# Optimization experiments

Measured on AMD Instinct MI355X. Metric: run time of the kernel, lower is better.

Reference implementation:

```python
import jax, jax.numpy as jnp
import numpy as np

B, S, H, NH = 2, 2048, 4096, 32
D = H // NH  # head_dim = 128
ROPE_THETA = 10000.0


def setup_inputs() -> dict:
    key = jax.random.key(0)
    k0, k1, k2 = jax.random.split(key, 3)
    hidden_states = jax.random.normal(k0, (B, S, H), dtype=jnp.float32) * 0.02
    w_pack = jax.random.normal(k1, (H, 3 * H), dtype=jnp.float32) * 0.02  # fused QKV weight
    w_o = jax.random.normal(k2, (H, H), dtype=jnp.float32) * 0.02         # o_proj weight
    positions = jnp.broadcast_to(jnp.arange(S, dtype=jnp.int32), (B, S))
    return {"positions": positions, "hidden_states": hidden_states, "w_pack": w_pack, "w_o": w_o}


def _rope(x, positions):
    # neox-style rotary embedding (vLLM get_rope default), x: [B, S, NH, D]
    half = D // 2
    inv_freq = 1.0 / (ROPE_THETA ** (jnp.arange(0, half, dtype=jnp.float32) * 2.0 / D))
    freqs = positions.astype(jnp.float32)[..., None] * inv_freq  # [B, S, half]
    cos = jnp.cos(freqs)[:, :, None, :]  # [B, S, 1, half]
    sin = jnp.sin(freqs)[:, :, None, :]
    x1, x2 = x[..., :half], x[..., half:]
    return jnp.concatenate([x1 * cos - x2 * sin, x2 * cos + x1 * sin], axis=-1)


def reference(positions, hidden_states, w_pack, w_o):
    # fused QKV projection
    qkv = jnp.einsum('bsh,hf->bsf', hidden_states, w_pack)
    q, k, v = jnp.split(qkv, 3, axis=-1)
    q = q.reshape(B, S, NH, D)
    k = k.reshape(B, S, NH, D)
    v = v.reshape(B, S, NH, D)
    # RoPE on q, k
    q = _rope(q, positions)
    k = _rope(k, positions)
    # causal scaled dot-product attention
    scale = D ** -0.5
    scores = jnp.einsum('bqhd,bkhd->bhqk', q, k) * scale  # [B, NH, S, S]
    causal = jnp.tril(jnp.ones((S, S), dtype=bool))
    scores = jnp.where(causal[None, None], scores, jnp.finfo(scores.dtype).min)
    probs = jax.nn.softmax(scores, axis=-1)
    out = jnp.einsum('bhqk,bkhd->bqhd', probs, v).reshape(B, S, H)
    # output projection
    return jnp.einsum('bsh,hf->bsf', out, w_o)
```

## Files before the change

### kernel.cpp

```cpp
#include <hip/hip_runtime.h>

#define Sdim   2048
#define Hdim   4096
#define NHEADS 32
#define Dh     128
#define Mrows  4096
#define QKVLD  12288

typedef __attribute__((ext_vector_type(8))) short short8;
typedef __attribute__((ext_vector_type(4))) float f32x4;
typedef __attribute__((ext_vector_type(4))) float float4v;

__device__ __forceinline__ short f2bf(float f) {
  union { float f; unsigned u; } x; x.f = f;
  unsigned r = x.u + 0x7fffu + ((x.u >> 16) & 1u);
  return (short)(r >> 16);
}
__device__ __forceinline__ float bf2f(short s) {
  union { unsigned u; float f; } x; x.u = ((unsigned)(unsigned short)s) << 16;
  return x.f;
}

__device__ __forceinline__ void gload_lds16(const void* g, void* l) {
  __builtin_amdgcn_global_load_lds(
      (const __attribute__((address_space(1))) void*)g,
      (__attribute__((address_space(3))) void*)l, 16, 0, 0);
}

__global__ void k_cvt(const float* __restrict__ src, short* __restrict__ dst, int n8) {
  int idx = blockIdx.x * blockDim.x + threadIdx.x;
  if (idx >= n8) return;
  const float4v* s = (const float4v*)src + (size_t)idx * 2;
  float4v a = s[0], b = s[1];
  short8 o;
  o[0] = f2bf(a.x); o[1] = f2bf(a.y); o[2] = f2bf(a.z); o[3] = f2bf(a.w);
  o[4] = f2bf(b.x); o[5] = f2bf(b.y); o[6] = f2bf(b.z); o[7] = f2bf(b.w);
  *((short8*)dst + idx) = o;
}

__global__ void k_tcvt64(const float* __restrict__ src, short* __restrict__ dst,
                         int R, int C) {
  __shared__ float t[64][65];
  const int tid = threadIdx.x;
  const int r0 = blockIdx.y * 64, c0 = blockIdx.x * 64;
  const int ir = tid >> 4, ic = (tid & 15) << 2;
#pragma unroll
  for (int p = 0; p < 4; ++p) {
    const float4v v = *(const float4v*)(src + (size_t)(r0 + p * 16 + ir) * C + c0 + ic);
    t[p * 16 + ir][ic] = v.x; t[p * 16 + ir][ic + 1] = v.y;
    t[p * 16 + ir][ic + 2] = v.z; t[p * 16 + ir][ic + 3] = v.w;
  }
  __syncthreads();
  const int oc = tid >> 3, orr = (tid & 7) << 3;
#pragma unroll
  for (int p = 0; p < 2; ++p) {
    int c = p * 32 + oc;
    short8 o;
#pragma unroll
    for (int j = 0; j < 8; ++j) o[j] = f2bf(t[orr + j][c]);
    *(short8*)(dst + (size_t)(c0 + c) * R + r0 + orr) = o;
  }
}

__device__ __forceinline__ void stage_half256(const short* G, int ld, int row0, int kcol,
                                              char* lds, int tid) {
#pragma unroll
  for (int j = 0; j < 2; ++j) {
    int p = j * 512 + tid;
    int r = p >> 3;
    int c = ((p & 7) ^ (r & 7)) << 3;
    gload_lds16(G + (size_t)(row0 + r) * ld + kcol + c,
                lds + ((j * 512 + (tid & 448)) << 4));
  }
}

#define MFMA_Q(qm, qn)                                                                   \
  do {                                                                                   \
    __builtin_amdgcn_s_setprio(1);                                                       \
    _Pragma("unroll")                                                                    \
    for (int m4 = 0; m4 < 4; ++m4)                                                       \
      _Pragma("unroll")                                                                  \
      for (int n2 = 0; n2 < 2; ++n2) {                                                   \
        acc[(qm)*4+m4][(qn)*2+n2] = __builtin_amdgcn_mfma_f32_16x16x32_bf16(             \
            av[m4][0], bv[(qn)*2+n2][0], acc[(qm)*4+m4][(qn)*2+n2], 0, 0, 0);            \
        acc[(qm)*4+m4][(qn)*2+n2] = __builtin_amdgcn_mfma_f32_16x16x32_bf16(             \
            av[m4][1], bv[(qn)*2+n2][1], acc[(qm)*4+m4][(qn)*2+n2], 0, 0, 0);            \
      }                                                                                  \
    __builtin_amdgcn_s_setprio(0);                                                       \
  } while (0)

#define PH_BARRIER()                    \
  do {                                  \
    __builtin_amdgcn_s_barrier();       \
    __builtin_amdgcn_sched_barrier(0);  \
  } while (0)

template<bool C_F32>
__global__ __launch_bounds__(512, 2) void k_gemm256(const short* __restrict__ A, int lda,
                                                    const short* __restrict__ Bt, int ldb,
                                                    void* __restrict__ Cp, int ldc,
                                                    int Ndim, int Kdim) {
  __shared__ __align__(16) char smem[131072];
  const int tid  = threadIdx.x;
  const int lane = tid & 63;
  const int wave = tid >> 6;
  const int lo = lane & 15, hi = lane >> 4;
  const int wr = wave >> 2, wc = wave & 3;

  const int nblk = gridDim.x;
  const int lid = (blockIdx.x & 7) * (nblk >> 3) + (blockIdx.x >> 3);
  const int nbn = Ndim >> 8;
  const int bm0 = (lid / nbn) << 8;
  const int bn0 = (lid % nbn) << 8;

  f32x4 acc[8][4];
#pragma unroll
  for (int i = 0; i < 8; ++i)
#pragma unroll
    for (int j = 0; j < 4; ++j) acc[i][j] = (f32x4){0.f, 0.f, 0.f, 0.f};

  short8 av[4][2], bv[4][2];
  const int swz = (lo & 7) << 4;
  const int brow = (wc & 1) * 64;

  stage_half256(Bt, ldb, bn0,       0, smem + 32768,         tid);
  stage_half256(Bt, ldb, bn0 + 128, 0, smem + 32768 + 16384, tid);
  stage_half256(A,  lda, bm0,       0, smem,                 tid);
  stage_half256(A,  lda, bm0 + 128, 0, smem + 16384,         tid);

  const int NK = Kdim >> 6;
  for (int kt = 0; kt < NK; ++kt) {
    const int cur = kt & 1;
    const char* Ab = smem + cur * 65536 + wr * 16384;
    const char* Bb = smem + cur * 65536 + 32768 + (wc >> 1) * 16384;
    char* nA = smem + (cur ^ 1) * 65536;
    char* nB = nA + 32768;
    const int kc = (kt + 1) << 6;
    const bool pf = (kt + 1 < NK);

    if (pf) {
      stage_half256(Bt, ldb, bn0,       kc, nB,         tid);
      stage_half256(Bt, ldb, bn0 + 128, kc, nB + 16384, tid);
      asm volatile("s_waitcnt vmcnt(4)" ::: "memory");
    } else {
      asm volatile("s_waitcnt vmcnt(0)" ::: "memory");
    }
    PH_BARRIER();
#pragma unroll
    for (int m4 = 0; m4 < 4; ++m4)
#pragma unroll
      for (int ks = 0; ks < 2; ++ks)
        av[m4][ks] = *(const short8*)(Ab + (m4 * 16 + lo) * 128 + ((ks * 64 + hi * 16) ^ swz));
#pragma unroll
    for (int ni = 0; ni < 2; ++ni)
#pragma unroll
      for (int ks = 0; ks < 2; ++ks)
        bv[ni][ks] = *(const short8*)(Bb + (brow + ni * 16 + lo) * 128 + ((ks * 64 + hi * 16) ^ swz));
    MFMA_Q(0, 0);
#pragma unroll
    for (int ni = 2; ni < 4; ++ni)
#pragma unroll
      for (int ks = 0; ks < 2; ++ks)
        bv[ni][ks] = *(const short8*)(Bb + (brow + ni * 16 + lo) * 128 + ((ks * 64 + hi * 16) ^ swz));

    if (pf) {
      stage_half256(A, lda, bm0,       kc, nA,         tid);
      stage_half256(A, lda, bm0 + 128, kc, nA + 16384, tid);
    }
    PH_BARRIER();
    MFMA_Q(0, 1);
#pragma unroll
    for (int m4 = 0; m4 < 4; ++m4)
#pragma unroll
      for (int ks = 0; ks < 2; ++ks)
        av[m4][ks] = *(const short8*)(Ab + ((64 + m4 * 16 + lo) * 128) + ((ks * 64 + hi * 16) ^ swz));

    PH_BARRIER();
    MFMA_Q(1, 0);

    PH_BARRIER();
    MFMA_Q(1, 1);
  }

#pragma unroll
  for (int mi = 0; mi < 8; ++mi)
#pragma unroll
    for (int r = 0; r < 4; ++r) {
      int row = bm0 + wr * 128 + mi * 16 + hi * 4 + r;
#pragma unroll
      for (int ni = 0; ni < 4; ++ni) {
        int col = bn0 + wc * 64 + ni * 16 + lo;
        if (C_F32) ((float*)Cp)[(size_t)row * ldc + col] = acc[mi][ni][r];
        else       ((short*)Cp)[(size_t)row * ldc + col] = f2bf(acc[mi][ni][r]);
      }
    }
}

__global__ void k_ropevt(short* __restrict__ qkv, const int* __restrict__ positions,
                         short* __restrict__ vt) {
  __shared__ short tile[4096];
  const int bid = blockIdx.x;
  const int tid = threadIdx.x;
  if (bid < 4096) {
    int idx = bid * 256 + tid;
    int t = idx & 7;
    int h = (idx >> 3) & 31;
    int row = idx >> 8;
    float pos = (float)positions[row];
    size_t o = (size_t)row * QKVLD + h * 128 + t * 8;
    short8 q1 = *(short8*)(qkv + o),        q2 = *(short8*)(qkv + o + 64);
    short8 k1 = *(short8*)(qkv + o + 4096), k2 = *(short8*)(qkv + o + 4160);
#pragma unroll
    for (int j = 0; j < 8; ++j) {
      int d = t * 8 + j;
      float inv = exp2f((float)d * -0.2076205059304570f);
      float ang = pos * inv, s, c;
      sincosf(ang, &s, &c);
      float a1 = bf2f(q1[j]), a2 = bf2f(q2[j]);
      q1[j] = f2bf(a1 * c - a2 * s); q2[j] = f2bf(a2 * c + a1 * s);
      float b1 = bf2f(k1[j]), b2 = bf2f(k2[j]);
      k1[j] = f2bf(b1 * c - b2 * s); k2[j] = f2bf(b2 * c + b1 * s);
    }
    *(short8*)(qkv + o) = q1;        *(short8*)(qkv + o + 64) = q2;
    *(short8*)(qkv + o + 4096) = k1; *(short8*)(qkv + o + 4160) = k2;
  } else {
    int idx = bid - 4096;
    const int c0 = (idx & 63) << 6;
    const int s0 = ((idx >> 6) & 31) << 6;
    const int b  = idx >> 11;
#pragma unroll
    for (int j = 0; j < 2; ++j) {
      int chunk = j * 256 + tid;
      int row = chunk >> 3, c8 = chunk & 7;
      short8 v = *(const short8*)(qkv + (size_t)(b * 2048 + s0 + row) * QKVLD + 8192 + c0 + c8 * 8);
      int sw = c8 ^ ((row ^ (row >> 3)) & 7);
      *(short8*)((char*)tile + row * 128 + sw * 16) = v;
    }
    __syncthreads();
#pragma unroll
    for (int j = 0; j < 2; ++j) {
      int chunk = j * 256 + tid;
      int d = chunk >> 3, s8 = (chunk & 7) << 3;
      short8 o;
#pragma unroll
      for (int j2 = 0; j2 < 8; ++j2) {
        int s = s8 + j2;
        int sw = ((d >> 3) ^ ((s ^ (s >> 3)) & 7));
        o[j2] = *(const short*)((const char*)tile + s * 128 + sw * 16 + (d & 7) * 2);
      }
      *(short8*)(vt + (size_t)(b * 4096 + c0 + d) * Sdim + s0 + s8) = o;
    }
  }
}

__device__ __forceinline__ void stage_kv(const short* Kb, const short* Vtb, int kv0,
                                         char* kbuf, char* vbuf, int tid, int wave) {
#pragma unroll
  for (int i = 0; i < 4; ++i) {
    int p = i * 256 + tid;
    int r = p >> 4;
    int c = (p & 15) ^ (r & 7);
    gload_lds16(Kb + (size_t)(kv0 + r) * QKVLD + (c << 3),
                kbuf + ((i * 256 + wave * 64) << 4));
  }
#pragma unroll
  for (int i = 0; i < 4; ++i) {
    int p = i * 256 + tid;
    int r = p >> 3;
    int c = (p & 7) ^ (r & 7);
    gload_lds16(Vtb + (size_t)r * Sdim + kv0 + (c << 3),
                vbuf + ((i * 256 + wave * 64) << 4));
  }
}

__global__ __launch_bounds__(256, 2) void k_attn(short* __restrict__ qkv,
                                                 const short* __restrict__ Vt,
                                                 const float* __restrict__ w_o,
                                                 short* __restrict__ Wot) {
  __shared__ __align__(16) char smem[81920];
  const int tid  = threadIdx.x;

  if (blockIdx.x >= 1024) {
    float (*t)[65] = (float(*)[65])smem;
    const int idx = blockIdx.x - 1024;
    const int c0 = (idx & 63) << 6, r0 = (idx >> 6) << 6;
    const int ir = tid >> 4, ic = (tid & 15) << 2;
#pragma unroll
    for (int p = 0; p < 4; ++p) {
      const float4v v = *(const float4v*)(w_o + (size_t)(r0 + p * 16 + ir) * 4096 + c0 + ic);
      t[p * 16 + ir][ic] = v.x; t[p * 16 + ir][ic + 1] = v.y;
      t[p * 16 + ir][ic + 2] = v.z; t[p * 16 + ir][ic + 3] = v.w;
    }
    __syncthreads();
    const int oc = tid >> 3, orr = (tid & 7) << 3;
#pragma unroll
    for (int p = 0; p < 2; ++p) {
      int c = p * 32 + oc;
      short8 o;
#pragma unroll
      for (int j = 0; j < 8; ++j) o[j] = f2bf(t[orr + j][c]);
      *(short8*)(Wot + (size_t)(c0 + c) * 4096 + r0 + orr) = o;
    }
    return;
  }

  const int lane = tid & 63;
  const int wave = tid >> 6;
  const int lo = lane & 15, hi = lane >> 4;

  const int bid = blockIdx.x;
  const int lid = (bid & 7) * 128 + (bid >> 3);
  const int bh = lid >> 4;
  const int qt = 15 - (lid & 15);
  const int b = bh >> 5, h = bh & 31;
  const int q0 = qt << 7;

  short* base = qkv + (size_t)b * Sdim * QKVLD;
  const short* Qb = base + h * Dh;
  const short* Kb = base + Hdim + h * Dh;
  const short* Vtb = Vt + (size_t)(b * 32 + h) * 128 * Sdim;
  const int qrow0 = q0 + wave * 32;

  short* Pw = (short*)(smem + 65536 + wave * 4096);

  const float SEXP = 0.088388347648318447f * 1.4426950408889634f;

  short8 qf[2][4];
#pragma unroll
  for (int mi = 0; mi < 2; ++mi)
#pragma unroll
    for (int ks = 0; ks < 4; ++ks) {
      qf[mi][ks] = *(const short8*)(Qb + (size_t)(qrow0 + mi * 16 + lo) * QKVLD + ks * 32 + hi * 8);
#pragma unroll
      for (int j = 0; j < 8; ++j)
        qf[mi][ks][j] = f2bf(bf2f(qf[mi][ks][j]) * SEXP);
    }

  f32x4 acc_o[2][9];
  float m_run[2][4];
#pragma unroll
  for (int mi = 0; mi < 2; ++mi) {
#pragma unroll
    for (int nf = 0; nf < 9; ++nf) acc_o[mi][nf] = (f32x4){0.f, 0.f, 0.f, 0.f};
#pragma unroll
    for (int r = 0; r < 4; ++r) m_run[mi][r] = -1e30f;
  }

  short8 vones;
#pragma unroll
  for (int j = 0; j < 8; ++j) vones[j] = (short)0x3F80;

  const int nkv = (q0 + 128) >> 6;
  const int swz = (lo & 7) << 4;

  stage_kv(Kb, Vtb, 0, smem, smem + 16384, tid, wave);
  __syncthreads();

  int cur = 0;
  for (int kvt = 0; kvt < nkv; ++kvt) {
    const int kv0 = kvt << 6;
    if (kvt + 1 < nkv)
      stage_kv(Kb, Vtb, kv0 + 64, smem + (cur ^ 1) * 32768,
               smem + (cur ^ 1) * 32768 + 16384, tid, wave);

    if (kv0 <= qrow0 + 31) {
      const char* kl = smem + cur * 32768;
      const char* vl = smem + cur * 32768 + 16384;

      f32x4 accs[2][4];
#pragma unroll
      for (int mi = 0; mi < 2; ++mi)
#pragma unroll
        for (int nf = 0; nf < 4; ++nf) accs[mi][nf] = (f32x4){0.f, 0.f, 0.f, 0.f};
#pragma unroll
      for (int ks = 0; ks < 4; ++ks) {
        short8 kf[4];
#pragma unroll
        for (int nf = 0; nf < 4; ++nf) {
          int r = nf * 16 + lo;
          kf[nf] = *(const short8*)(kl + r * 256 + ((ks * 64 + hi * 16) ^ swz));
        }
        __builtin_amdgcn_s_setprio(1);
#pragma unroll
        for (int mi = 0; mi < 2; ++mi)
#pragma unroll
          for (int nf = 0; nf < 4; ++nf)
            accs[mi][nf] = __builtin_amdgcn_mfma_f32_16x16x32_bf16(qf[mi][ks], kf[nf], accs[mi][nf], 0, 0, 0);
        __builtin_amdgcn_s_setprio(0);
      }

      const bool needmask = (kv0 + 63 > qrow0);
      float pmax[2][4];
      bool okall = true;
#pragma unroll
      for (int mi = 0; mi < 2; ++mi) {
#pragma unroll
        for (int r = 0; r < 4; ++r) {
          const int qrow = qrow0 + mi * 16 + hi * 4 + r;
          if (needmask) {
#pragma unroll
            for (int nf = 0; nf < 4; ++nf) {
              int col = kv0 + nf * 16 + lo;
              accs[mi][nf][r] = (col <= qrow) ? accs[mi][nf][r] : -1e30f;
            }
          }
          float tmax = fmaxf(fmaxf(accs[mi][0][r], accs[mi][1][r]),
                             fmaxf(accs[mi][2][r], accs[mi][3][r]));
#pragma unroll
          for (int off = 1; off < 16; off <<= 1)
            tmax = fmaxf(tmax, __shfl_xor(tmax, off, 64));
          pmax[mi][r] = tmax;
          okall = okall && (tmax <= m_run[mi][r] + 8.0f);
        }
      }
      if (!__all(okall)) {
#pragma unroll
        for (int mi = 0; mi < 2; ++mi)
#pragma unroll
          for (int r = 0; r < 4; ++r) {
            float mnew = fmaxf(m_run[mi][r], pmax[mi][r]);
            float alpha = exp2f(m_run[mi][r] - mnew);
            m_run[mi][r] = mnew;
#pragma unroll
            for (int nf = 0; nf < 9; ++nf) acc_o[mi][nf][r] *= alpha;
          }
      }
#pragma unroll
      for (int mi = 0; mi < 2; ++mi)
#pragma unroll
        for (int r = 0; r < 4; ++r) {
          const int prow = mi * 16 + hi * 4 + r;
          const int psw = prow & 7;
#pragma unroll
          for (int nf = 0; nf < 4; ++nf) {
            float p = exp2f(accs[mi][nf][r] - m_run[mi][r]);
            int col = nf * 16 + lo;
            Pw[(prow << 6) + (((col >> 3) ^ psw) << 3) + (col & 7)] = f2bf(p);
          }
        }

#pragma unroll
      for (int ks = 0; ks < 2; ++ks) {
        short8 pf[2];
#pragma unroll
        for (int mi = 0; mi < 2; ++mi) {
          int prow = mi * 16 + lo;
          pf[mi] = *(const short8*)((const char*)Pw + prow * 128 + (((ks * 4 + hi) ^ (prow & 7)) << 4));
        }
        __builtin_amdgcn_s_setprio(1);
#pragma unroll
        for (int nf = 0; nf < 9; ++nf) {
          short8 vf;
          if (nf < 8) {
            int row = nf * 16 + lo;
            vf = *(const short8*)(vl + row * 128 + ((ks * 64 + hi * 16) ^ swz));
          } else {
            vf = vones;
          }
#pragma unroll
          for (int mi = 0; mi < 2; ++mi)
            acc_o[mi][nf] = __builtin_amdgcn_mfma_f32_16x16x32_bf16(pf[mi], vf, acc_o[mi][nf], 0, 0, 0);
        }
        __builtin_amdgcn_s_setprio(0);
      }
    }

    __syncthreads();
    cur ^= 1;
  }

  short* Osm = (short*)smem;
#pragma unroll
  for (int mi = 0; mi < 2; ++mi)
#pragma unroll
    for (int r = 0; r < 4; ++r) {
      float inv = 1.0f / acc_o[mi][8][r];
      int row = wave * 32 + mi * 16 + hi * 4 + r;
#pragma unroll
      for (int nf = 0; nf < 8; ++nf)
        Osm[row * 128 + nf * 16 + lo] = f2bf(acc_o[mi][nf][r] * inv);
    }
  __syncthreads();
  short* Ob = base + h * Dh;
#pragma unroll
  for (int it = 0; it < 8; ++it) {
    int chunk = it * 256 + tid;
    int row = chunk >> 4, c8 = chunk & 15;
    *(short8*)(Ob + (size_t)(q0 + row) * QKVLD + c8 * 8) =
        *(const short8*)(Osm + row * 128 + c8 * 8);
  }
}

extern "C" void kernel_launch(void* const* d_in, const int* in_sizes, int n_in,
                              void* d_out, int out_size, void* d_ws, size_t ws_size,
                              hipStream_t stream) {
  const int*   positions = (const int*)d_in[0];
  const float* hidden    = (const float*)d_in[1];
  const float* w_pack    = (const float*)d_in[2];
  const float* w_o       = (const float*)d_in[3];
  float* out = (float*)d_out;

  char* ws = (char*)d_ws;
  short* Wpt  = (short*)ws;
  short* qkvb = (short*)(ws + (size_t)12288 * 4096 * 2);
  short* Wot  = (short*)ws;
  short* Hbf  = (short*)d_out;
  short* Vtg  = (short*)((char*)d_out + ((size_t)32 << 20));

  k_cvt<<<8192, 256, 0, stream>>>(hidden, Hbf, 4096 * 4096 / 8);
  k_tcvt64<<<dim3(12288 / 64, 4096 / 64), 256, 0, stream>>>(w_pack, Wpt, 4096, 12288);
  k_gemm256<false><<<dim3(768), 512, 0, stream>>>(Hbf, 4096, Wpt, 4096, qkvb, QKVLD, 12288, 4096);
  k_ropevt<<<8192, 256, 0, stream>>>(qkvb, positions, Vtg);
  k_attn<<<dim3(5120), 256, 0, stream>>>(qkvb, Vtg, w_o, Wot);
  k_gemm256<true><<<dim3(256), 512, 0, stream>>>(qkvb, QKVLD, Wot, 4096, out, 4096, 4096, 4096);
}
```

Before: 744.8 us.

## Fuse RoPE and V transpose into the QKV GEMM epilogue

Removes the separate RoPE/V-transpose kernel. The QKV GEMM now applies the rotary embedding in its epilogue and writes V transposed straight to the Vt buffer. To make this possible, each wave's B-tile column mapping changes so that a lane holds the d and d+64 pair of a head together. This saves a full read-modify-write pass over the qkv buffer and one kernel launch. In exchange, the transposed V stores are strided 8-byte writes, the epilogue adds sincos work, and the changed column interleave may affect LDS bank behaviour.

```diff
diff --git a/kernel.cpp b/kernel.cpp
--- a/kernel.cpp
+++ b/kernel.cpp
@@ -8,6 +8,7 @@
 #define QKVLD  12288
 
 typedef __attribute__((ext_vector_type(8))) short short8;
+typedef __attribute__((ext_vector_type(4))) short short4v;
 typedef __attribute__((ext_vector_type(4))) float f32x4;
 typedef __attribute__((ext_vector_type(4))) float float4v;
 
@@ -95,11 +96,13 @@
     __builtin_amdgcn_sched_barrier(0);  \
   } while (0)
 
-template<bool C_F32>
+template<int MODE>
 __global__ __launch_bounds__(512, 2) void k_gemm256(const short* __restrict__ A, int lda,
                                                     const short* __restrict__ Bt, int ldb,
                                                     void* __restrict__ Cp, int ldc,
-                                                    int Ndim, int Kdim) {
+                                                    int Ndim, int Kdim,
+                                                    const int* __restrict__ positions,
+                                                    short* __restrict__ Vtg) {
   __shared__ __align__(16) char smem[131072];
   const int tid  = threadIdx.x;
   const int lane = tid & 63;
@@ -121,7 +124,6 @@
 
   short8 av[4][2], bv[4][2];
   const int swz = (lo & 7) << 4;
-  const int brow = (wc & 1) * 64;
 
   stage_half256(Bt, ldb, bn0,       0, smem + 32768,         tid);
   stage_half256(Bt, ldb, bn0 + 128, 0, smem + 32768 + 16384, tid);
@@ -132,7 +134,7 @@
   for (int kt = 0; kt < NK; ++kt) {
     const int cur = kt & 1;
     const char* Ab = smem + cur * 65536 + wr * 16384;
-    const char* Bb = smem + cur * 65536 + 32768 + (wc >> 1) * 16384;
+    const char* Bb = smem + cur * 65536 + 32768;
     char* nA = smem + (cur ^ 1) * 65536;
     char* nB = nA + 32768;
     const int kc = (kt + 1) << 6;
@@ -155,13 +157,13 @@
     for (int ni = 0; ni < 2; ++ni)
 #pragma unroll
       for (int ks = 0; ks < 2; ++ks)
-        bv[ni][ks] = *(const short8*)(Bb + (brow + ni * 16 + lo) * 128 + ((ks * 64 + hi * 16) ^ swz));
+        bv[ni][ks] = *(const short8*)(Bb + (wc * 16 + ni * 64 + lo) * 128 + ((ks * 64 + hi * 16) ^ swz));
     MFMA_Q(0, 0);
 #pragma unroll
     for (int ni = 2; ni < 4; ++ni)
 #pragma unroll
       for (int ks = 0; ks < 2; ++ks)
-        bv[ni][ks] = *(const short8*)(Bb + (brow + ni * 16 + lo) * 128 + ((ks * 64 + hi * 16) ^ swz));
+        bv[ni][ks] = *(const short8*)(Bb + (wc * 16 + ni * 64 + lo) * 128 + ((ks * 64 + hi * 16) ^ swz));
 
     if (pf) {
       stage_half256(A, lda, bm0,       kc, nA,         tid);
@@ -182,74 +184,52 @@
     MFMA_Q(1, 1);
   }
 
-#pragma unroll
-  for (int mi = 0; mi < 8; ++mi)
-#pragma unroll
-    for (int r = 0; r < 4; ++r) {
-      int row = bm0 + wr * 128 + mi * 16 + hi * 4 + r;
+  if (MODE == 0) {
+#pragma unroll
+    for (int mi = 0; mi < 8; ++mi)
+#pragma unroll
+      for (int r = 0; r < 4; ++r) {
+        int row = bm0 + wr * 128 + mi * 16 + hi * 4 + r;
+#pragma unroll
+        for (int ni = 0; ni < 4; ++ni) {
+          int col = bn0 + wc * 16 + ni * 64 + lo;
+          ((float*)Cp)[(size_t)row * ldc + col] = acc[mi][ni][r];
+        }
+      }
+  } else if (bn0 < 8192) {
+    short* qkvb = (short*)Cp;
+    const int dd = wc * 16 + lo;
+    const float inv = exp2f((float)dd * -0.2076205059304570f);
+#pragma unroll
+    for (int mi = 0; mi < 8; ++mi)
+#pragma unroll
+      for (int r = 0; r < 4; ++r) {
+        int row = bm0 + wr * 128 + mi * 16 + hi * 4 + r;
+        float pos = (float)positions[row];
+        float s, c;
+        sincosf(pos * inv, &s, &c);
+        size_t base = (size_t)row * ldc + bn0 + wc * 16 + lo;
+        float x1 = acc[mi][0][r], x2 = acc[mi][1][r];
+        qkvb[base]       = f2bf(x1 * c - x2 * s);
+        qkvb[base + 64]  = f2bf(x2 * c + x1 * s);
+        float x3 = acc[mi][2][r], x4 = acc[mi][3][r];
+        qkvb[base + 128] = f2bf(x3 * c - x4 * s);
+        qkvb[base + 192] = f2bf(x4 * c + x3 * s);
+      }
+  } else {
+    const int b = bm0 >> 11;
+    const int s0 = (bm0 & 2047) + wr * 128;
+#pragma unroll
+    for (int mi = 0; mi < 8; ++mi)
 #pragma unroll
       for (int ni = 0; ni < 4; ++ni) {
-        int col = bn0 + wc * 64 + ni * 16 + lo;
-        if (C_F32) ((float*)Cp)[(size_t)row * ldc + col] = acc[mi][ni][r];
-        else       ((short*)Cp)[(size_t)row * ldc + col] = f2bf(acc[mi][ni][r]);
-      }
-    }
-}
-
-__global__ void k_ropevt(short* __restrict__ qkv, const int* __restrict__ positions,
-                         short* __restrict__ vt) {
-  __shared__ short tile[4096];
-  const int bid = blockIdx.x;
-  const int tid = threadIdx.x;
-  if (bid < 4096) {
-    int idx = bid * 256 + tid;
-    int t = idx & 7;
-    int h = (idx >> 3) & 31;
-    int row = idx >> 8;
-    float pos = (float)positions[row];
-    size_t o = (size_t)row * QKVLD + h * 128 + t * 8;
-    short8 q1 = *(short8*)(qkv + o),        q2 = *(short8*)(qkv + o + 64);
-    short8 k1 = *(short8*)(qkv + o + 4096), k2 = *(short8*)(qkv + o + 4160);
-#pragma unroll
-    for (int j = 0; j < 8; ++j) {
-      int d = t * 8 + j;
-      float inv = exp2f((float)d * -0.2076205059304570f);
-      float ang = pos * inv, s, c;
-      sincosf(ang, &s, &c);
-      float a1 = bf2f(q1[j]), a2 = bf2f(q2[j]);
-      q1[j] = f2bf(a1 * c - a2 * s); q2[j] = f2bf(a2 * c + a1 * s);
-      float b1 = bf2f(k1[j]), b2 = bf2f(k2[j]);
-      k1[j] = f2bf(b1 * c - b2 * s); k2[j] = f2bf(b2 * c + b1 * s);
-    }
-    *(short8*)(qkv + o) = q1;        *(short8*)(qkv + o + 64) = q2;
-    *(short8*)(qkv + o + 4096) = k1; *(short8*)(qkv + o + 4160) = k2;
-  } else {
-    int idx = bid - 4096;
-    const int c0 = (idx & 63) << 6;
-    const int s0 = ((idx >> 6) & 31) << 6;
-    const int b  = idx >> 11;
-#pragma unroll
-    for (int j = 0; j < 2; ++j) {
-      int chunk = j * 256 + tid;
-      int row = chunk >> 3, c8 = chunk & 7;
-      short8 v = *(const short8*)(qkv + (size_t)(b * 2048 + s0 + row) * QKVLD + 8192 + c0 + c8 * 8);
-      int sw = c8 ^ ((row ^ (row >> 3)) & 7);
-      *(short8*)((char*)tile + row * 128 + sw * 16) = v;
-    }
-    __syncthreads();
-#pragma unroll
-    for (int j = 0; j < 2; ++j) {
-      int chunk = j * 256 + tid;
-      int d = chunk >> 3, s8 = (chunk & 7) << 3;
-      short8 o;
-#pragma unroll
-      for (int j2 = 0; j2 < 8; ++j2) {
-        int s = s8 + j2;
-        int sw = ((d >> 3) ^ ((s ^ (s >> 3)) & 7));
-        o[j2] = *(const short*)((const char*)tile + s * 128 + sw * 16 + (d & 7) * 2);
-      }
-      *(short8*)(vt + (size_t)(b * 4096 + c0 + d) * Sdim + s0 + s8) = o;
-    }
+        int col = bn0 - 8192 + wc * 16 + ni * 64 + lo;
+        int h = col >> 7, d = col & 127;
+        short4v o;
+#pragma unroll
+        for (int r = 0; r < 4; ++r) o[r] = f2bf(acc[mi][ni][r]);
+        *(short4v*)(Vtg + (size_t)((b * 32 + h) * 128 + d) * Sdim + s0 + mi * 16 + hi * 4) = o;
+      }
   }
 }
 
@@ -509,8 +489,9 @@
 
   k_cvt<<<8192, 256, 0, stream>>>(hidden, Hbf, 4096 * 4096 / 8);
   k_tcvt64<<<dim3(12288 / 64, 4096 / 64), 256, 0, stream>>>(w_pack, Wpt, 4096, 12288);
-  k_gemm256<false><<<dim3(768), 512, 0, stream>>>(Hbf, 4096, Wpt, 4096, qkvb, QKVLD, 12288, 4096);
-  k_ropevt<<<8192, 256, 0, stream>>>(qkvb, positions, Vtg);
+  k_gemm256<1><<<dim3(768), 512, 0, stream>>>(Hbf, 4096, Wpt, 4096, qkvb, QKVLD, 12288, 4096,
+                                              positions, Vtg);
   k_attn<<<dim3(5120), 256, 0, stream>>>(qkvb, Vtg, w_o, Wot);
-  k_gemm256<true><<<dim3(256), 512, 0, stream>>>(qkvb, QKVLD, Wot, 4096, out, 4096, 4096, 4096);
-}
+  k_gemm256<0><<<dim3(256), 512, 0, stream>>>(qkvb, QKVLD, Wot, 4096, out, 4096, 4096, 4096,
+                                              nullptr, nullptr);
+}
```

Result: faster. 728.8 us (-2.1%).
